# Optimization experiments

Hardware: AMD Instinct MI355X
Metric: run time of the kernel (lower is better)

## Reference

```python
import jax, jax.numpy as jnp
import numpy as np

N_NODES = 100000
N_EDGES = 3200000
IN_CH = 256
OUT_CH = 1


def setup_inputs() -> dict:
    key = jax.random.key(0)
    ks = jax.random.split(key, 8)
    x = jax.random.normal(ks[0], (N_NODES, IN_CH), dtype=jnp.float32)
    edge_index = jax.random.randint(ks[1], (2, N_EDGES), 0, N_NODES, dtype=jnp.int64 if jax.config.jax_enable_x64 else jnp.int32)
    s_in = 1.0 / np.sqrt(IN_CH)
    Wq = jax.random.uniform(ks[2], (IN_CH, OUT_CH), jnp.float32, -s_in, s_in)
    bq = jax.random.uniform(ks[3], (OUT_CH,), jnp.float32, -s_in, s_in)
    Wk = jax.random.uniform(ks[4], (IN_CH, OUT_CH), jnp.float32, -s_in, s_in)
    bk = jax.random.uniform(ks[5], (OUT_CH,), jnp.float32, -s_in, s_in)
    Wv = jax.random.uniform(ks[6], (IN_CH, IN_CH), jnp.float32, -s_in, s_in)
    bv = jax.random.uniform(ks[7], (IN_CH,), jnp.float32, -s_in, s_in)
    return {"x": x, "edge_index": edge_index, "Wq": Wq, "bq": bq,
            "Wk": Wk, "bk": bk, "Wv": Wv, "bv": bv}


def reference(x, edge_index, Wq, bq, Wk, bk, Wv, bv):
    num_nodes = x.shape[0]
    q = x @ Wq + bq                       # [N, out_ch]
    k = x @ Wk + bk                       # [N, out_ch]
    v = x @ Wv + bv                       # [N, in_ch]
    row, col = edge_index[0], edge_index[1]
    # edge attention logits: gather + dot over out_ch
    att = jnp.sum(q[row] * k[col], axis=-1)          # [E]
    att = jax.nn.leaky_relu(att, negative_slope=0.2)
    att = jax.nn.softmax(att, axis=0)                # softmax over ALL edges (dim=0)
    # scatter-add edge attention to source nodes
    attention_weights = jax.ops.segment_sum(att, row, num_segments=num_nodes)  # [N]
    graph_emb = jnp.sum(attention_weights[:, None] * v, axis=0)                # [in_ch]
    return graph_emb, attention_weights
```

## Files before the change

### kernel.cpp

```cpp
#include <hip/hip_runtime.h>

#define N_NODES 100000
#define N_EDGES 3200000
#define CH 256

#define EPB_S 8192
#define GS 391
#define NB2 25
#define BSZ 4096
#define G_AGG 10
#define SLICE 40
#define GRID_QK 1563
#define GRID_POOL 512
#define YCOPY 16

#define OFF_TOTAL  0
#define OFF_PTOT   16
#define OFF_YU16   528
#define OFF_PRE    4624
#define OFF_Q      14800
#define OFF_K      114800
#define OFF_AWU    214800
#define OFF_PART   314800
#define OFF_EX     1338800
#define OFF_ROW    4541872

__global__ __launch_bounds__(256) void k_qk(const float* __restrict__ x,
                                            const float* __restrict__ Wq,
                                            const float* __restrict__ bq,
                                            const float* __restrict__ Wk,
                                            const float* __restrict__ bk,
                                            float* __restrict__ q,
                                            float* __restrict__ k,
                                            float* __restrict__ yu16) {
    int t = threadIdx.x;
    if (blockIdx.x < 16) yu16[blockIdx.x * 256 + t] = 0.0f;
    int w = t >> 6, lane = t & 63;
    int g = lane >> 4, seg = lane & 15;
    float4 wq4[4], wk4[4];
    #pragma unroll
    for (int j = 0; j < 4; ++j) {
        wq4[j] = ((const float4*)Wq)[seg + 16 * j];
        wk4[j] = ((const float4*)Wk)[seg + 16 * j];
    }
    float bqs = bq[0], bks = bk[0];
    int base = blockIdx.x * 64 + w * 16 + g;
    #pragma unroll
    for (int i = 0; i < 4; ++i) {
        int n = base + i * 4;
        if (n < N_NODES) {
            const float4* xr = (const float4*)(x + (size_t)n * CH);
            float dq = 0.0f, dk = 0.0f;
            #pragma unroll
            for (int j = 0; j < 4; ++j) {
                float4 xv = xr[seg + 16 * j];
                dq = fmaf(xv.x, wq4[j].x, fmaf(xv.y, wq4[j].y,
                     fmaf(xv.z, wq4[j].z, fmaf(xv.w, wq4[j].w, dq))));
                dk = fmaf(xv.x, wk4[j].x, fmaf(xv.y, wk4[j].y,
                     fmaf(xv.z, wk4[j].z, fmaf(xv.w, wk4[j].w, dk))));
            }
            dq += __shfl_down(dq, 8); dq += __shfl_down(dq, 4);
            dq += __shfl_down(dq, 2); dq += __shfl_down(dq, 1);
            dk += __shfl_down(dk, 8); dk += __shfl_down(dk, 4);
            dk += __shfl_down(dk, 2); dk += __shfl_down(dk, 1);
            if (seg == 0) { q[n] = dq + bqs; k[n] = dk + bks; }
        }
    }
}

__global__ __launch_bounds__(512) void k_sort(const int* __restrict__ ei,
                                              const float* __restrict__ q,
                                              const float* __restrict__ k,
                                              float* __restrict__ ex_out,
                                              unsigned short* __restrict__ row_out,
                                              int* __restrict__ pre) {
    __shared__ int cnt[8][NB2];
    __shared__ int base8[8][NB2];
    __shared__ int pref[NB2 + 1];
    __shared__ int bsum[NB2];
    __shared__ float lex[EPB_S];
    __shared__ unsigned short lrow[EPB_S];
    int t = threadIdx.x, blk = blockIdx.x, w = t >> 6;
    int e0 = blk * EPB_S;
    int ecnt = min(EPB_S, N_EDGES - e0);
    for (int i = t; i < 8 * NB2; i += 512) ((int*)cnt)[i] = 0;
    __syncthreads();
    int rr[16]; float ee[16];
    #pragma unroll
    for (int j = 0; j < 16; ++j) {
        int i = j * 512 + t;
        if (i < ecnt) {
            int r = ei[e0 + i], c = ei[N_EDGES + e0 + i];
            float v = q[r] * k[c];
            v = (v >= 0.0f) ? v : 0.2f * v;
            rr[j] = r; ee[j] = __expf(v);
            atomicAdd(&cnt[w][r >> 12], 1);
        } else rr[j] = -1;
    }
    __syncthreads();
    if (t < NB2) {
        int s = 0;
        #pragma unroll
        for (int ww = 0; ww < 8; ++ww) { base8[ww][t] = s; s += cnt[ww][t]; }
        bsum[t] = s;
    }
    __syncthreads();
    if (t == 0) {
        int run = 0;
        #pragma unroll
        for (int b = 0; b < NB2; ++b) { pref[b] = run; run += bsum[b]; }
        pref[NB2] = run;
    }
    __syncthreads();
    if (t < 8 * NB2) {
        int ww = t / NB2, b = t - ww * NB2;
        base8[ww][b] += pref[b];
    }
    if (t < NB2 + 1) pre[blk * 26 + t] = pref[t];
    __syncthreads();
    #pragma unroll
    for (int j = 0; j < 16; ++j) {
        if (rr[j] >= 0) {
            int b = rr[j] >> 12;
            int p = atomicAdd(&base8[w][b], 1);
            lex[p] = ee[j];
            lrow[p] = (unsigned short)(rr[j] & (BSZ - 1));
        }
    }
    __syncthreads();
    size_t gb = (size_t)blk * EPB_S;
    for (int i = t; i < ecnt; i += 512) ex_out[gb + i] = lex[i];
    unsigned* ro = (unsigned*)(row_out + gb);
    const unsigned* lr = (const unsigned*)lrow;
    int words = (ecnt + 1) >> 1;
    for (int i = t; i < words; i += 512) ro[i] = lr[i];
}

__global__ __launch_bounds__(512) void k_agg(const float* __restrict__ ex,
                                             const unsigned short* __restrict__ row,
                                             const int* __restrict__ pre,
                                             float* __restrict__ partial) {
    int b = blockIdx.x / G_AGG, g = blockIdx.x % G_AGG;
    __shared__ float acc[BSZ];
    int t = threadIdx.x, w = t >> 6, lane = t & 63;
    for (int i = t; i < BSZ; i += 512) acc[i] = 0.0f;
    __syncthreads();
    int sb0 = g * SLICE, sb1 = min(sb0 + SLICE, GS);
    for (int sb = sb0 + w; sb < sb1; sb += 8) {
        size_t gbase = (size_t)sb * EPB_S;
        int s0 = pre[sb * 26 + b], s1 = pre[sb * 26 + b + 1];
        for (int i = s0 + lane; i < s1; i += 64)
            atomicAdd(&acc[row[gbase + i]], ex[gbase + i]);
    }
    __syncthreads();
    float* dst = partial + ((size_t)b * G_AGG + g) * BSZ;
    for (int i = t; i < BSZ; i += 512) dst[i] = acc[i];
}

__global__ __launch_bounds__(256) void k_fold(const float* __restrict__ partial,
                                              float* __restrict__ awu,
                                              float* __restrict__ ptot) {
    int t = threadIdx.x;
    int n = blockIdx.x * 256 + t;
    float s = 0.0f;
    if (n < N_NODES) {
        int b = n >> 12, off = n & (BSZ - 1);
        const float* p = partial + (size_t)b * G_AGG * BSZ + off;
        #pragma unroll
        for (int g = 0; g < G_AGG; ++g) s += p[(size_t)g * BSZ];
        awu[n] = s;
    }
    float r = s;
    #pragma unroll
    for (int off = 32; off; off >>= 1) r += __shfl_down(r, off);
    __shared__ float sm[4];
    if ((t & 63) == 0) sm[t >> 6] = r;
    __syncthreads();
    if (t == 0) ptot[blockIdx.x] = sm[0] + sm[1] + sm[2] + sm[3];
}

__global__ __launch_bounds__(256) void k_pool(const float* __restrict__ x,
                                              const float* __restrict__ awu,
                                              const float* __restrict__ ptot,
                                              float* __restrict__ totalp,
                                              float* __restrict__ yu16,
                                              float* __restrict__ aw_out) {
    int t = threadIdx.x, s = t >> 6, g = t & 63;
    float ts = ptot[t] + ((t + 256 < GS) ? ptot[t + 256] : 0.0f);
    #pragma unroll
    for (int off = 32; off; off >>= 1) ts += __shfl_down(ts, off);
    __shared__ float sm[4];
    __shared__ float tot;
    if (g == 0) sm[s] = ts;
    __syncthreads();
    if (t == 0) {
        tot = sm[0] + sm[1] + sm[2] + sm[3];
        if (blockIdx.x == 0) totalp[0] = tot;
    }
    __syncthreads();
    float inv = 1.0f / tot;

    const float4* X4 = (const float4*)x;
    float4 acc = make_float4(0.f, 0.f, 0.f, 0.f);
    for (int base = blockIdx.x * 8; base < N_NODES; base += GRID_POOL * 8) {
        float a0 = awu[base + s];
        float a1 = awu[base + 4 + s];
        float4 x0 = X4[(size_t)(base + s) * 64 + g];
        float4 x1 = X4[(size_t)(base + 4 + s) * 64 + g];
        acc.x = fmaf(a0, x0.x, acc.x); acc.y = fmaf(a0, x0.y, acc.y);
        acc.z = fmaf(a0, x0.z, acc.z); acc.w = fmaf(a0, x0.w, acc.w);
        acc.x = fmaf(a1, x1.x, acc.x); acc.y = fmaf(a1, x1.y, acc.y);
        acc.z = fmaf(a1, x1.z, acc.z); acc.w = fmaf(a1, x1.w, acc.w);
    }
    __shared__ float4 tmp4[4][64];
    tmp4[s][g] = acc;
    __syncthreads();
    const float* tmp = (const float*)tmp4;
    float sum = tmp[0 * 256 + t] + tmp[1 * 256 + t] + tmp[2 * 256 + t] + tmp[3 * 256 + t];
    atomicAdd(&yu16[(blockIdx.x & (YCOPY - 1)) * 256 + t], sum);
    for (int i = blockIdx.x * 256 + t; i < N_NODES; i += GRID_POOL * 256)
        aw_out[i] = awu[i] * inv;
}

__global__ __launch_bounds__(256) void k_final(const float* __restrict__ yu16,
                                               const float* __restrict__ totalp,
                                               const float* __restrict__ Wv,
                                               const float* __restrict__ bv,
                                               float* __restrict__ out) {
    __shared__ float ysh[256];
    __shared__ float red[256];
    int t = threadIdx.x;
    float inv = 1.0f / totalp[0];
    float yv = 0.0f;
    #pragma unroll
    for (int j = 0; j < YCOPY; ++j) yv += yu16[j * 256 + t];
    ysh[t] = yv * inv;
    __syncthreads();
    int c = blockIdx.x * 32 + (t & 31), rg = t >> 5;
    float acc = 0.0f;
    #pragma unroll
    for (int j = 0; j < 32; ++j) {
        int kk = rg * 32 + j;
        acc = fmaf(ysh[kk], Wv[(size_t)kk * CH + c], acc);
    }
    red[t] = acc;
    __syncthreads();
    if (t < 32) {
        float sv = 0.0f;
        #pragma unroll
        for (int j = 0; j < 8; ++j) sv += red[j * 32 + t];
        out[blockIdx.x * 32 + t] = sv + bv[blockIdx.x * 32 + t];
    }
}

extern "C" void kernel_launch(void* const* d_in, const int* in_sizes, int n_in,
                              void* d_out, int out_size, void* d_ws, size_t ws_size,
                              hipStream_t stream) {
    const float* x  = (const float*)d_in[0];
    const int*   ei = (const int*)d_in[1];
    const float* Wq = (const float*)d_in[2];
    const float* bq = (const float*)d_in[3];
    const float* Wk = (const float*)d_in[4];
    const float* bk = (const float*)d_in[5];
    const float* Wv = (const float*)d_in[6];
    const float* bv = (const float*)d_in[7];
    float* out = (float*)d_out;
    float* ws  = (float*)d_ws;

    float*          totalp  = ws + OFF_TOTAL;
    float*          ptot    = ws + OFF_PTOT;
    float*          yu16    = ws + OFF_YU16;
    int*            pre     = (int*)(ws + OFF_PRE);
    float*          q       = ws + OFF_Q;
    float*          k       = ws + OFF_K;
    float*          awu     = ws + OFF_AWU;
    float*          partial = ws + OFF_PART;
    float*          ex      = ws + OFF_EX;
    unsigned short* row     = (unsigned short*)(ws + OFF_ROW);

    hipLaunchKernelGGL(k_qk, dim3(GRID_QK), dim3(256), 0, stream,
                       x, Wq, bq, Wk, bk, q, k, yu16);
    hipLaunchKernelGGL(k_sort, dim3(GS), dim3(512), 0, stream,
                       ei, q, k, ex, row, pre);
    hipLaunchKernelGGL(k_agg, dim3(NB2 * G_AGG), dim3(512), 0, stream,
                       ex, row, pre, partial);
    hipLaunchKernelGGL(k_fold, dim3((N_NODES + 255) / 256), dim3(256), 0, stream,
                       partial, awu, ptot);
    hipLaunchKernelGGL(k_pool, dim3(GRID_POOL), dim3(256), 0, stream,
                       x, awu, ptot, totalp, yu16, out + CH);
    hipLaunchKernelGGL(k_final, dim3(8), dim3(256), 0, stream,
                       yu16, totalp, Wv, bv, out);
}
```

Baseline: 270.7 us.

## Replace bucket-sort edge aggregation with direct global float atomics

Removes the three-kernel pipeline (local bucket sort, per-bucket shared-memory aggregation, fold) and replaces it with one edge kernel. Each thread handles four edges, computes exp of the leaky-relu logit and scatters it into the node array with unsafe (hardware fast) float atomics, while the softmax denominator is reduced per block and added atomically to a global total. Zeroing of the accumulators moves into the q/k kernel. This cuts intermediate traffic and two launches, but puts 3.2M random global atomics on L2 and makes the sums depend on atomic ordering.

Result: slower. 366.2 us (+35.3%).

```diff
diff --git a/kernel.cpp b/kernel.cpp
--- a/kernel.cpp
+++ b/kernel.cpp
@@ -4,26 +4,16 @@
 #define N_EDGES 3200000
 #define CH 256
 
-#define EPB_S 8192
-#define GS 391
-#define NB2 25
-#define BSZ 4096
-#define G_AGG 10
-#define SLICE 40
 #define GRID_QK 1563
+#define GRID_E  3125
 #define GRID_POOL 512
 #define YCOPY 16
 
-#define OFF_TOTAL  0
-#define OFF_PTOT   16
-#define OFF_YU16   528
-#define OFF_PRE    4624
-#define OFF_Q      14800
-#define OFF_K      114800
-#define OFF_AWU    214800
-#define OFF_PART   314800
-#define OFF_EX     1338800
-#define OFF_ROW    4541872
+#define OFF_TOTAL 0
+#define OFF_YU16  16
+#define OFF_Q     4112
+#define OFF_K     104112
+#define OFF_AWU   204112
 
 __global__ __launch_bounds__(256) void k_qk(const float* __restrict__ x,
                                             const float* __restrict__ Wq,
@@ -32,9 +22,14 @@
                                             const float* __restrict__ bk,
                                             float* __restrict__ q,
                                             float* __restrict__ k,
-                                            float* __restrict__ yu16) {
+                                            float* __restrict__ yu16,
+                                            float* __restrict__ awu,
+                                            float* __restrict__ totalp) {
     int t = threadIdx.x;
+    int gid = blockIdx.x * 256 + t;
     if (blockIdx.x < 16) yu16[blockIdx.x * 256 + t] = 0.0f;
+    if (gid < N_NODES) awu[gid] = 0.0f;
+    if (gid == 0) totalp[0] = 0.0f;
     int w = t >> 6, lane = t & 63;
     int g = lane >> 4, seg = lane & 15;
     float4 wq4[4], wk4[4];
@@ -68,137 +63,43 @@
     }
 }
 
-__global__ __launch_bounds__(512) void k_sort(const int* __restrict__ ei,
+__global__ __launch_bounds__(256) void k_edge(const int* __restrict__ ei,
                                               const float* __restrict__ q,
                                               const float* __restrict__ k,
-                                              float* __restrict__ ex_out,
-                                              unsigned short* __restrict__ row_out,
-                                              int* __restrict__ pre) {
-    __shared__ int cnt[8][NB2];
-    __shared__ int base8[8][NB2];
-    __shared__ int pref[NB2 + 1];
-    __shared__ int bsum[NB2];
-    __shared__ float lex[EPB_S];
-    __shared__ unsigned short lrow[EPB_S];
-    int t = threadIdx.x, blk = blockIdx.x, w = t >> 6;
-    int e0 = blk * EPB_S;
-    int ecnt = min(EPB_S, N_EDGES - e0);
-    for (int i = t; i < 8 * NB2; i += 512) ((int*)cnt)[i] = 0;
+                                              float* __restrict__ awu,
+                                              float* __restrict__ totalp) {
+    int t = threadIdx.x;
+    int i0 = (blockIdx.x * 256 + t) * 4;
+    const int4 r4 = *(const int4*)(ei + i0);
+    const int4 c4 = *(const int4*)(ei + N_EDGES + i0);
+    float q0 = q[r4.x], q1 = q[r4.y], q2 = q[r4.z], q3 = q[r4.w];
+    float k0 = k[c4.x], k1 = k[c4.y], k2 = k[c4.z], k3 = k[c4.w];
+    float v0 = q0 * k0, v1 = q1 * k1, v2 = q2 * k2, v3 = q3 * k3;
+    v0 = (v0 >= 0.0f) ? v0 : 0.2f * v0;
+    v1 = (v1 >= 0.0f) ? v1 : 0.2f * v1;
+    v2 = (v2 >= 0.0f) ? v2 : 0.2f * v2;
+    v3 = (v3 >= 0.0f) ? v3 : 0.2f * v3;
+    float e0 = __expf(v0), e1 = __expf(v1), e2 = __expf(v2), e3 = __expf(v3);
+    unsafeAtomicAdd(&awu[r4.x], e0);
+    unsafeAtomicAdd(&awu[r4.y], e1);
+    unsafeAtomicAdd(&awu[r4.z], e2);
+    unsafeAtomicAdd(&awu[r4.w], e3);
+    float ts = (e0 + e1) + (e2 + e3);
+    #pragma unroll
+    for (int off = 32; off; off >>= 1) ts += __shfl_down(ts, off);
+    __shared__ float sm[4];
+    if ((t & 63) == 0) sm[t >> 6] = ts;
     __syncthreads();
-    int rr[16]; float ee[16];
-    #pragma unroll
-    for (int j = 0; j < 16; ++j) {
-        int i = j * 512 + t;
-        if (i < ecnt) {
-            int r = ei[e0 + i], c = ei[N_EDGES + e0 + i];
-            float v = q[r] * k[c];
-            v = (v >= 0.0f) ? v : 0.2f * v;
-            rr[j] = r; ee[j] = __expf(v);
-            atomicAdd(&cnt[w][r >> 12], 1);
-        } else rr[j] = -1;
-    }
-    __syncthreads();
-    if (t < NB2) {
-        int s = 0;
-        #pragma unroll
-        for (int ww = 0; ww < 8; ++ww) { base8[ww][t] = s; s += cnt[ww][t]; }
-        bsum[t] = s;
-    }
-    __syncthreads();
-    if (t == 0) {
-        int run = 0;
-        #pragma unroll
-        for (int b = 0; b < NB2; ++b) { pref[b] = run; run += bsum[b]; }
-        pref[NB2] = run;
-    }
-    __syncthreads();
-    if (t < 8 * NB2) {
-        int ww = t / NB2, b = t - ww * NB2;
-        base8[ww][b] += pref[b];
-    }
-    if (t < NB2 + 1) pre[blk * 26 + t] = pref[t];
-    __syncthreads();
-    #pragma unroll
-    for (int j = 0; j < 16; ++j) {
-        if (rr[j] >= 0) {
-            int b = rr[j] >> 12;
-            int p = atomicAdd(&base8[w][b], 1);
-            lex[p] = ee[j];
-            lrow[p] = (unsigned short)(rr[j] & (BSZ - 1));
-        }
-    }
-    __syncthreads();
-    size_t gb = (size_t)blk * EPB_S;
-    for (int i = t; i < ecnt; i += 512) ex_out[gb + i] = lex[i];
-    unsigned* ro = (unsigned*)(row_out + gb);
-    const unsigned* lr = (const unsigned*)lrow;
-    int words = (ecnt + 1) >> 1;
-    for (int i = t; i < words; i += 512) ro[i] = lr[i];
-}
-
-__global__ __launch_bounds__(512) void k_agg(const float* __restrict__ ex,
-                                             const unsigned short* __restrict__ row,
-                                             const int* __restrict__ pre,
-                                             float* __restrict__ partial) {
-    int b = blockIdx.x / G_AGG, g = blockIdx.x % G_AGG;
-    __shared__ float acc[BSZ];
-    int t = threadIdx.x, w = t >> 6, lane = t & 63;
-    for (int i = t; i < BSZ; i += 512) acc[i] = 0.0f;
-    __syncthreads();
-    int sb0 = g * SLICE, sb1 = min(sb0 + SLICE, GS);
-    for (int sb = sb0 + w; sb < sb1; sb += 8) {
-        size_t gbase = (size_t)sb * EPB_S;
-        int s0 = pre[sb * 26 + b], s1 = pre[sb * 26 + b + 1];
-        for (int i = s0 + lane; i < s1; i += 64)
-            atomicAdd(&acc[row[gbase + i]], ex[gbase + i]);
-    }
-    __syncthreads();
-    float* dst = partial + ((size_t)b * G_AGG + g) * BSZ;
-    for (int i = t; i < BSZ; i += 512) dst[i] = acc[i];
-}
-
-__global__ __launch_bounds__(256) void k_fold(const float* __restrict__ partial,
-                                              float* __restrict__ awu,
-                                              float* __restrict__ ptot) {
-    int t = threadIdx.x;
-    int n = blockIdx.x * 256 + t;
-    float s = 0.0f;
-    if (n < N_NODES) {
-        int b = n >> 12, off = n & (BSZ - 1);
-        const float* p = partial + (size_t)b * G_AGG * BSZ + off;
-        #pragma unroll
-        for (int g = 0; g < G_AGG; ++g) s += p[(size_t)g * BSZ];
-        awu[n] = s;
-    }
-    float r = s;
-    #pragma unroll
-    for (int off = 32; off; off >>= 1) r += __shfl_down(r, off);
-    __shared__ float sm[4];
-    if ((t & 63) == 0) sm[t >> 6] = r;
-    __syncthreads();
-    if (t == 0) ptot[blockIdx.x] = sm[0] + sm[1] + sm[2] + sm[3];
+    if (t == 0) unsafeAtomicAdd(totalp, (sm[0] + sm[1]) + (sm[2] + sm[3]));
 }
 
 __global__ __launch_bounds__(256) void k_pool(const float* __restrict__ x,
                                               const float* __restrict__ awu,
-                                              const float* __restrict__ ptot,
-                                              float* __restrict__ totalp,
+                                              const float* __restrict__ totalp,
                                               float* __restrict__ yu16,
                                               float* __restrict__ aw_out) {
     int t = threadIdx.x, s = t >> 6, g = t & 63;
-    float ts = ptot[t] + ((t + 256 < GS) ? ptot[t + 256] : 0.0f);
-    #pragma unroll
-    for (int off = 32; off; off >>= 1) ts += __shfl_down(ts, off);
-    __shared__ float sm[4];
-    __shared__ float tot;
-    if (g == 0) sm[s] = ts;
-    __syncthreads();
-    if (t == 0) {
-        tot = sm[0] + sm[1] + sm[2] + sm[3];
-        if (blockIdx.x == 0) totalp[0] = tot;
-    }
-    __syncthreads();
-    float inv = 1.0f / tot;
+    float inv = 1.0f / totalp[0];
 
     const float4* X4 = (const float4*)x;
     float4 acc = make_float4(0.f, 0.f, 0.f, 0.f);
@@ -217,7 +118,7 @@
     __syncthreads();
     const float* tmp = (const float*)tmp4;
     float sum = tmp[0 * 256 + t] + tmp[1 * 256 + t] + tmp[2 * 256 + t] + tmp[3 * 256 + t];
-    atomicAdd(&yu16[(blockIdx.x & (YCOPY - 1)) * 256 + t], sum);
+    unsafeAtomicAdd(&yu16[(blockIdx.x & (YCOPY - 1)) * 256 + t], sum);
     for (int i = blockIdx.x * 256 + t; i < N_NODES; i += GRID_POOL * 256)
         aw_out[i] = awu[i] * inv;
 }
@@ -267,27 +168,18 @@
     float* out = (float*)d_out;
     float* ws  = (float*)d_ws;
 
-    float*          totalp  = ws + OFF_TOTAL;
-    float*          ptot    = ws + OFF_PTOT;
-    float*          yu16    = ws + OFF_YU16;
-    int*            pre     = (int*)(ws + OFF_PRE);
-    float*          q       = ws + OFF_Q;
-    float*          k       = ws + OFF_K;
-    float*          awu     = ws + OFF_AWU;
-    float*          partial = ws + OFF_PART;
-    float*          ex      = ws + OFF_EX;
-    unsigned short* row     = (unsigned short*)(ws + OFF_ROW);
+    float* totalp = ws + OFF_TOTAL;
+    float* yu16   = ws + OFF_YU16;
+    float* q      = ws + OFF_Q;
+    float* k      = ws + OFF_K;
+    float* awu    = ws + OFF_AWU;
 
     hipLaunchKernelGGL(k_qk, dim3(GRID_QK), dim3(256), 0, stream,
-                       x, Wq, bq, Wk, bk, q, k, yu16);
-    hipLaunchKernelGGL(k_sort, dim3(GS), dim3(512), 0, stream,
-                       ei, q, k, ex, row, pre);
-    hipLaunchKernelGGL(k_agg, dim3(NB2 * G_AGG), dim3(512), 0, stream,
-                       ex, row, pre, partial);
-    hipLaunchKernelGGL(k_fold, dim3((N_NODES + 255) / 256), dim3(256), 0, stream,
-                       partial, awu, ptot);
+                       x, Wq, bq, Wk, bk, q, k, yu16, awu, totalp);
+    hipLaunchKernelGGL(k_edge, dim3(GRID_E), dim3(256), 0, stream,
+                       ei, q, k, awu, totalp);
     hipLaunchKernelGGL(k_pool, dim3(GRID_POOL), dim3(256), 0, stream,
-                       x, awu, ptot, totalp, yu16, out + CH);
+                       x, awu, totalp, yu16, out + CH);
     hipLaunchKernelGGL(k_final, dim3(8), dim3(256), 0, stream,
                        yu16, totalp, Wv, bv, out);
 }
```
